# Kernel tuning notes

Measured on AMD Instinct MI355X. Metric: run time of the kernel, lower is better.

Reference implementation:

```python
import jax, jax.numpy as jnp
import numpy as np

T, A, F, E_FEAT = 64, 16, 4, 64
E = F * E_FEAT          # 256 lattice embed dim
H_ENC = 256             # encoder LSTM hidden (per direction)
D_IN = 256              # input token embed dim
DEC_HID = 2 * H_ENC     # decoder hidden = concat(fwd,bwd) encoder hidden
D_ATTN = 256
V_LAT, V_IN = 20000, 100000
NEG = jnp.float32(-1e10)
DEC_LAYERS = 2


def setup_inputs() -> dict:
    key = jax.random.key(0)
    ks = jax.random.split(key, 20)
    def gn(k, shape, scale=0.05):
        return jax.random.normal(k, shape, dtype=jnp.float32) * scale
    inp = {}
    inp['lattice'] = jax.random.randint(ks[0], (1, T, A, F), 0, V_LAT, dtype=jnp.int32)
    inp['analysis_lengths'] = jnp.full((1, T), A, dtype=jnp.int32)
    inp['inputs'] = jax.random.randint(ks[1], (1, T), 0, V_IN, dtype=jnp.int32)
    inp['input_lengths'] = jnp.full((1, 1, 1), T, dtype=jnp.int32)
    inp['gold_indices'] = jax.random.randint(ks[2], (1, T), 0, A, dtype=jnp.int32)
    inp['sos_ids'] = jax.random.randint(ks[3], (F,), 0, V_LAT, dtype=jnp.int32)
    inp['lat_emb_table'] = gn(ks[4], (V_LAT, E_FEAT))
    inp['in_emb_table'] = gn(ks[5], (V_IN, D_IN))
    # encoder biLSTM: 2 layers x 2 directions (PyTorch gate order i,f,g,o)
    inp['enc_Wih0'] = gn(ks[6], (2, 4 * H_ENC, E))
    inp['enc_Whh0'] = gn(ks[7], (2, 4 * H_ENC, H_ENC))
    inp['enc_b0'] = gn(ks[8], (2, 4 * H_ENC))
    inp['enc_Wih1'] = gn(ks[9], (2, 4 * H_ENC, 2 * H_ENC))
    inp['enc_Whh1'] = gn(ks[10], (2, 4 * H_ENC, H_ENC))
    inp['enc_b1'] = gn(ks[11], (2, 4 * H_ENC))
    # decoder LSTM: 2 layers, input = E + D_IN == DEC_HID
    inp['dec_Wih'] = gn(ks[12], (DEC_LAYERS, 4 * DEC_HID, E + D_IN))
    inp['dec_Whh'] = gn(ks[13], (DEC_LAYERS, 4 * DEC_HID, DEC_HID))
    inp['dec_b'] = gn(ks[14], (DEC_LAYERS, 4 * DEC_HID))
    # additive pointer attention
    inp['attn_Wq'] = gn(ks[15], (DEC_HID, D_ATTN))
    inp['attn_Wk'] = gn(ks[16], (DEC_HID, D_ATTN))
    inp['attn_v'] = gn(ks[17], (D_ATTN,))
    return inp


def _lstm_cell(x, h, c, Wih, Whh, b):
    g = x @ Wih.T + h @ Whh.T + b
    i, f, gg, o = jnp.split(g, 4, axis=-1)
    c = jax.nn.sigmoid(f) * c + jax.nn.sigmoid(i) * jnp.tanh(gg)
    h = jax.nn.sigmoid(o) * jnp.tanh(c)
    return h, c


def _lstm_layer(xs, Wih, Whh, b, reverse):
    h0 = jnp.zeros((Whh.shape[-1],), xs.dtype)
    def step(carry, x):
        h, c = _lstm_cell(x, carry[0], carry[1], Wih, Whh, b)
        return (h, c), h
    (hT, cT), ys = jax.lax.scan(step, (h0, h0), xs, reverse=reverse)
    return ys, hT, cT


def reference(lattice, analysis_lengths, inputs, input_lengths, gold_indices, sos_ids,
              lat_emb_table, in_emb_table,
              enc_Wih0, enc_Whh0, enc_b0, enc_Wih1, enc_Whh1, enc_b1,
              dec_Wih, dec_Whh, dec_b, attn_Wq, attn_Wk, attn_v):
    # embed lattice: per-feature lookup, flatten feature embeds -> [1,T,A,E]
    emb_lat = lat_emb_table[lattice].reshape(1, T, A, E)
    # pack full lattice (analysis_lengths == A) into one sequence [T*A, E]
    x = emb_lat[0].reshape(T * A, E)
    # encoder biLSTM layer 0
    yf, hf0, cf0 = _lstm_layer(x, enc_Wih0[0], enc_Whh0[0], enc_b0[0], False)
    yb, hb0, cb0 = _lstm_layer(x, enc_Wih0[1], enc_Whh0[1], enc_b0[1], True)
    y = jnp.concatenate([yf, yb], axis=-1)
    # encoder biLSTM layer 1
    yf, hf1, cf1 = _lstm_layer(y, enc_Wih1[0], enc_Whh1[0], enc_b1[0], False)
    yb, hb1, cb1 = _lstm_layer(y, enc_Wih1[1], enc_Whh1[1], enc_b1[1], True)
    enc = jnp.concatenate([yf, yb], axis=-1).reshape(T, A, DEC_HID)
    # decoder init hidden: concat fwd/bwd final states per layer (matches the
    # view/transpose/reshape in forward_lattice_encode)
    h_dec = jnp.stack([jnp.concatenate([hf0, hb0]), jnp.concatenate([hf1, hb1])])
    c_dec = jnp.stack([jnp.concatenate([cf0, cb0]), jnp.concatenate([cf1, cb1])])
    sos_emb = lat_emb_table[sos_ids].reshape(E)
    tok_emb = in_emb_table[inputs[0]]      # [T, D_IN]
    lat_seq = emb_lat[0]                   # [T, A, E]
    gold = gold_indices[0]                 # [T] teacher forcing
    alens = analysis_lengths[0]            # [T]
    col = jnp.arange(A)

    def step(carry, xs):
        h, c, prev = carry
        enc_t, tok_t, lat_t, g_t, len_t = xs
        inp_t = jnp.concatenate([prev, tok_t])   # [E + D_IN]
        hs, cs = [], []
        for l in range(DEC_LAYERS):
            hl, cl = _lstm_cell(inp_t, h[l], c[l], dec_Wih[l], dec_Whh[l], dec_b[l])
            hs.append(hl); cs.append(cl)
            inp_t = hl
        att = jnp.tanh(enc_t @ attn_Wk + inp_t @ attn_Wq) @ attn_v   # [A]
        scores = jnp.where(col < len_t, att, NEG)
        return (jnp.stack(hs), jnp.stack(cs), lat_t[g_t]), scores

    _, scores = jax.lax.scan(step, (h_dec, c_dec, sos_emb), (enc, tok_emb, lat_seq, gold, alens))
    return scores[None]  # [1, T, A]
```

## Files before the change

### kernel.cpp

```cpp
#include <hip/hip_runtime.h>
#include <math.h>

#define T_STEPS 64
#define A_DIM   16
#define SEQ     1024
#define HE      256
#define DH      512
#define GE      1024
#define GD      2048

typedef _Float16 h2_t __attribute__((ext_vector_type(2)));

__device__ __forceinline__ float sigf(float x) { return 1.f / (1.f + __expf(-x)); }
__device__ __forceinline__ float tanh_fast(float x) {
    float e = __expf(-2.f * x);
    return (1.f - e) / (1.f + e);
}

__device__ __forceinline__ float fdot2f(h2_t a, h2_t b, float c) {
#if defined(__has_builtin) && __has_builtin(__builtin_amdgcn_fdot2)
    return __builtin_amdgcn_fdot2(a, b, c, false);
#else
    return c + (float)a.x * (float)b.x + (float)a.y * (float)b.y;
#endif
}

__device__ __forceinline__ float poll_comm(const float* p) {
    float v;
    do {
        v = __hip_atomic_load(p, __ATOMIC_RELAXED, __HIP_MEMORY_SCOPE_AGENT);
    } while (v == 0.f);
    return v - 4.0f;
}

__device__ __forceinline__ void post_comm(float* p, float h) {
    __hip_atomic_store(p, h + 4.0f, __ATOMIC_RELAXED, __HIP_MEMORY_SCOPE_AGENT);
}

__global__ void k_embed(const int* __restrict__ lattice, const int* __restrict__ inputs,
                        const int* __restrict__ gold, const int* __restrict__ sos,
                        const float* __restrict__ lat_emb, const float* __restrict__ in_emb,
                        float* __restrict__ x, float* __restrict__ decin)
{
    int idx = blockIdx.x * 256 + threadIdx.x;
    if (idx < SEQ * 256) {
        int row = idx >> 8, e = idx & 255;
        int f = e >> 6, eo = e & 63;
        int id = lattice[row * 4 + f];
        x[idx] = lat_emb[id * 64 + eo];
    } else {
        int k = idx - SEQ * 256;
        if (k < T_STEPS * 512) {
            int t = k >> 9, d = k & 511;
            float val;
            if (d < 256) {
                int f = d >> 6, eo = d & 63;
                int id = (t == 0) ? sos[f]
                                  : lattice[(((t - 1) * A_DIM) + gold[t - 1]) * 4 + f];
                val = lat_emb[id * 64 + eo];
            } else {
                val = in_emb[inputs[t] * 256 + (d - 256)];
            }
            decin[k] = val;
        }
    }
}

__global__ __launch_bounds__(256) void k_gemm(
    const float* __restrict__ A, int lda, long sA,
    const float* __restrict__ B, int ldbn, int ldbk, long sB,
    const float* __restrict__ bias, int sBias,
    float* __restrict__ C, int ldc, long sC,
    int M, int N, int K)
{
    int b = blockIdx.z;
    A += b * sA; B += b * sB; C += b * sC;
    if (bias) bias += (long)b * sBias;
    int n0 = blockIdx.x * 64, m0 = blockIdx.y * 64;
    __shared__ float As[64][17];
    __shared__ float Bs[64][17];
    int tid = threadIdx.x;
    int tn = tid & 15, tm = tid >> 4;
    float acc[4][4] = {};
    int lk = tid & 15, lr = tid >> 4;
    for (int k0 = 0; k0 < K; k0 += 16) {
#pragma unroll
        for (int i = 0; i < 4; i++) {
            int row = lr + i * 16;
            int am = m0 + row;
            As[row][lk] = (am < M) ? A[(long)am * lda + k0 + lk] : 0.f;
            int bn = n0 + row;
            Bs[row][lk] = (bn < N) ? B[(long)bn * ldbn + (long)(k0 + lk) * ldbk] : 0.f;
        }
        __syncthreads();
#pragma unroll
        for (int k = 0; k < 16; k++) {
            float av[4], bv[4];
#pragma unroll
            for (int i = 0; i < 4; i++) av[i] = As[tm * 4 + i][k];
#pragma unroll
            for (int j = 0; j < 4; j++) bv[j] = Bs[tn * 4 + j][k];
#pragma unroll
            for (int i = 0; i < 4; i++)
#pragma unroll
                for (int j = 0; j < 4; j++) acc[i][j] += av[i] * bv[j];
        }
        __syncthreads();
    }
#pragma unroll
    for (int i = 0; i < 4; i++) {
        int m = m0 + tm * 4 + i;
        if (m >= M) continue;
#pragma unroll
        for (int j = 0; j < 4; j++) {
            int n = n0 + tn * 4 + j;
            if (n < N) C[(long)m * ldc + n] = acc[i][j] + (bias ? bias[n] : 0.f);
        }
    }
}

__global__ __launch_bounds__(256, 1) void k_rec_enc(
    const float* __restrict__ pre,
    const float* __restrict__ Whh,
    float* __restrict__ y,
    float* __restrict__ hfin,
    float* __restrict__ cfin,
    float* __restrict__ comm)
{
    const int tid = threadIdx.x, bid = blockIdx.x;
    const int r = bid & 3, dir = bid >> 2;
    const bool fwd = (dir == 0);
    const int jj = tid & 63, j = r * 64 + jj;
    const int row = (tid >> 6) * HE + j;
    const float* pre_d = pre + (long)dir * SEQ * GE;
    float* comm_d = comm + (long)dir * SEQ * HE;

    h2_t w2[128];
    {
        const float4* wr = (const float4*)(Whh + (long)dir * GE * HE + (long)row * HE);
#pragma unroll
        for (int i = 0; i < 64; i++) {
            float4 v = wr[i];
            w2[2 * i]     = h2_t{(_Float16)v.x, (_Float16)v.y};
            w2[2 * i + 1] = h2_t{(_Float16)v.z, (_Float16)v.w};
        }
    }

    __shared__ __align__(16) _Float16 hsArr[HE];
    __shared__ float gl[256];
    hsArr[tid] = (_Float16)0.f;
    __syncthreads();

    float c = 0.f, h_cur = 0.f;
    float pre_cur = pre_d[(long)(fwd ? 0 : SEQ - 1) * GE + row];

    for (int s = 0; s < SEQ; s++) {
        const int t = fwd ? s : SEQ - 1 - s;
        float acc = 0.f;
        const float4* hv = (const float4*)hsArr;
#pragma unroll
        for (int kk = 0; kk < 32; kk++) {
            float4 blk = hv[kk];
            const h2_t* hp = (const h2_t*)&blk;
            acc = fdot2f(w2[4 * kk + 0], hp[0], acc);
            acc = fdot2f(w2[4 * kk + 1], hp[1], acc);
            acc = fdot2f(w2[4 * kk + 2], hp[2], acc);
            acc = fdot2f(w2[4 * kk + 3], hp[3], acc);
        }
        gl[tid] = pre_cur + acc;
        if (s + 1 < SEQ) pre_cur = pre_d[(long)(fwd ? t + 1 : t - 1) * GE + row];
        __syncthreads();
        if (tid < 64) {
            float gi = gl[jj], gf = gl[64 + jj], gg = gl[128 + jj], go = gl[192 + jj];
            c = sigf(gf) * c + sigf(gi) * tanh_fast(gg);
            h_cur = sigf(go) * tanh_fast(c);
            post_comm(&comm_d[(long)t * HE + j], h_cur);
            y[(long)t * 512 + dir * HE + j] = h_cur;
            hsArr[j] = (_Float16)h_cur;
        }
        if (s + 1 < SEQ && tid < 192) {
            int idx = (r * 64 + 64 + tid) & 255;
            hsArr[idx] = (_Float16)poll_comm(&comm_d[(long)t * HE + idx]);
        }
        __syncthreads();
    }
    if (tid < 64) {
        hfin[dir * HE + j] = h_cur;
        cfin[dir * HE + j] = c;
    }
}

__global__ __launch_bounds__(256, 1) void k_rec_dec(
    const float* __restrict__ pre,
    const float* __restrict__ Whh,
    const float* __restrict__ hinit,
    const float* __restrict__ cinit,
    float* __restrict__ hseq,
    float* __restrict__ comm)
{
    const int tid = threadIdx.x, r = blockIdx.x;
    const int kh = tid >> 7, rem = tid & 127;
    const int q = rem >> 5, jj = rem & 31;
    const int row = q * DH + r * 32 + jj;
    const int k0 = kh * 256;

    h2_t w2[128];
    {
        const float4* wr = (const float4*)(Whh + (long)row * DH + k0);
#pragma unroll
        for (int i = 0; i < 64; i++) {
            float4 v = wr[i];
            w2[2 * i]     = h2_t{(_Float16)v.x, (_Float16)v.y};
            w2[2 * i + 1] = h2_t{(_Float16)v.z, (_Float16)v.w};
        }
    }

    __shared__ __align__(16) _Float16 hsArr[DH];
    __shared__ float part[256];
    __shared__ float gate[128];
    hsArr[tid] = (_Float16)hinit[tid];
    hsArr[tid + 256] = (_Float16)hinit[tid + 256];
    float c = (tid < 32) ? cinit[r * 32 + tid] : 0.f;
    float pre_cur = (tid < 128) ? pre[row] : 0.f;
    float h_cur = 0.f;
    __syncthreads();

    for (int s = 0; s < T_STEPS; s++) {
        float acc = 0.f;
        const float4* hv = (const float4*)(hsArr + k0);
#pragma unroll
        for (int kk = 0; kk < 32; kk++) {
            float4 blk = hv[kk];
            const h2_t* hp = (const h2_t*)&blk;
            acc = fdot2f(w2[4 * kk + 0], hp[0], acc);
            acc = fdot2f(w2[4 * kk + 1], hp[1], acc);
            acc = fdot2f(w2[4 * kk + 2], hp[2], acc);
            acc = fdot2f(w2[4 * kk + 3], hp[3], acc);
        }
        part[tid] = acc;
        __syncthreads();
        if (tid < 128) {
            float g = part[tid] + part[tid + 128] + pre_cur;
            if (s + 1 < T_STEPS) pre_cur = pre[(long)(s + 1) * GD + row];
            gate[tid] = g;
        }
        __syncthreads();
        if (tid < 32) {
            int jg = r * 32 + tid;
            float gi = gate[tid], gf = gate[32 + tid], gg = gate[64 + tid], go = gate[96 + tid];
            c = sigf(gf) * c + sigf(gi) * tanh_fast(gg);
            h_cur = sigf(go) * tanh_fast(c);
            post_comm(&comm[(long)s * DH + jg], h_cur);
            hseq[(long)s * DH + jg] = h_cur;
            hsArr[jg] = (_Float16)h_cur;
        }
        if (s + 1 < T_STEPS) {
            if (tid < 224) {
                int idx = (r * 32 + 32 + tid) & 511;
                hsArr[idx] = (_Float16)poll_comm(&comm[(long)s * DH + idx]);
            }
            {
                int idx = (r * 32 + 256 + tid) & 511;
                hsArr[idx] = (_Float16)poll_comm(&comm[(long)s * DH + idx]);
            }
        }
        __syncthreads();
    }
}

__global__ void k_attn(const float* __restrict__ encK, const float* __restrict__ qs,
                       const float* __restrict__ v, const int* __restrict__ alens,
                       float* __restrict__ out)
{
    int t = blockIdx.x;
    int tid = threadIdx.x;
    int wave = tid >> 6, lane = tid & 63;
    int len = alens[t];
    const float* qt = qs + t * 256;
    for (int a = wave; a < A_DIM; a += 4) {
        const float* ek = encK + (long)(t * A_DIM + a) * 256;
        float sum = 0.f;
#pragma unroll
        for (int e = 0; e < 4; e++) {
            int d = lane * 4 + e;
            sum += v[d] * tanhf(ek[d] + qt[d]);
        }
        for (int off = 32; off; off >>= 1) sum += __shfl_down(sum, off, 64);
        if (lane == 0) out[t * A_DIM + a] = (a < len) ? sum : -1e10f;
    }
}

extern "C" void kernel_launch(void* const* d_in, const int* in_sizes, int n_in,
                              void* d_out, int out_size, void* d_ws, size_t ws_size,
                              hipStream_t stream)
{
    (void)in_sizes; (void)n_in; (void)out_size; (void)ws_size;
    const int*   lattice = (const int*)d_in[0];
    const int*   alens   = (const int*)d_in[1];
    const int*   inputs  = (const int*)d_in[2];
    const int*   gold    = (const int*)d_in[4];
    const int*   sos     = (const int*)d_in[5];
    const float* lat_emb = (const float*)d_in[6];
    const float* in_emb  = (const float*)d_in[7];
    const float* Wih0    = (const float*)d_in[8];
    const float* Whh0    = (const float*)d_in[9];
    const float* b0      = (const float*)d_in[10];
    const float* Wih1    = (const float*)d_in[11];
    const float* Whh1    = (const float*)d_in[12];
    const float* b1      = (const float*)d_in[13];
    const float* dWih    = (const float*)d_in[14];
    const float* dWhh    = (const float*)d_in[15];
    const float* db      = (const float*)d_in[16];
    const float* Wq      = (const float*)d_in[17];
    const float* Wk      = (const float*)d_in[18];
    const float* av      = (const float*)d_in[19];
    float* out = (float*)d_out;
    float* ws  = (float*)d_ws;

    float* comm  = ws;
    float* commD = ws + 524288;
    float* xbuf  = ws + 589824;
    float* dpre  = xbuf;
    float* h0seq = xbuf + 131072;
    float* h1seq = xbuf + 163840;
    float* qseq  = xbuf + 196608;
    float* pre   = ws + 851968;
    float* y0    = ws + 2949120;
    float* hdec  = ws + 3473408;
    float* cdec  = ws + 3474432;
    float* decin = ws + 3475456;
    float* encK  = ws + 3508224;

    hipMemsetAsync(ws, 0, (524288 + 65536) * sizeof(float), stream);

    k_embed<<<1152, 256, 0, stream>>>(lattice, inputs, gold, sos, lat_emb, in_emb, xbuf, decin);

    k_gemm<<<dim3(16, 16, 2), 256, 0, stream>>>(
        xbuf, 256, 0L, Wih0, 256, 1, (long)GE * 256, b0, GE,
        pre, GE, (long)SEQ * GE, SEQ, GE, 256);
    k_rec_enc<<<8, 256, 0, stream>>>(pre, Whh0, y0, hdec, cdec, comm);

    hipMemsetAsync(comm, 0, 524288 * sizeof(float), stream);

    k_gemm<<<dim3(16, 16, 2), 256, 0, stream>>>(
        y0, 512, 0L, Wih1, 512, 1, (long)GE * 512, b1, GE,
        pre, GE, (long)SEQ * GE, SEQ, GE, 512);
    k_rec_enc<<<8, 256, 0, stream>>>(pre, Whh1, y0, hdec + 512, cdec + 512, comm);

    k_gemm<<<dim3(4, 16, 1), 256, 0, stream>>>(
        y0, 512, 0L, Wk, 1, 256, 0L, nullptr, 0,
        encK, 256, 0L, SEQ, 256, 512);

    k_gemm<<<dim3(32, 1, 1), 256, 0, stream>>>(
        decin, 512, 0L, dWih, 512, 1, 0L, db, 0,
        dpre, GD, 0L, T_STEPS, GD, 512);
    k_rec_dec<<<16, 256, 0, stream>>>(dpre, dWhh, hdec, cdec, h0seq, commD);

    k_gemm<<<dim3(32, 1, 1), 256, 0, stream>>>(
        h0seq, 512, 0L, dWih + (long)GD * 512, 512, 1, 0L, db + GD, 0,
        dpre, GD, 0L, T_STEPS, GD, 512);
    k_rec_dec<<<16, 256, 0, stream>>>(dpre, dWhh + (long)GD * 512, hdec + 512, cdec + 512,
                                      h1seq, commD + 32768);

    k_gemm<<<dim3(4, 1, 1), 256, 0, stream>>>(
        h1seq, 512, 0L, Wq, 1, 256, 0L, nullptr, 0,
        qseq, 256, 0L, T_STEPS, 256, 512);

    k_attn<<<64, 256, 0, stream>>>(encK, qseq, av, alens, out);
}
```

Before: 3.964 ms.

## Run each encoder LSTM direction in one 1024-thread block, dropping cross-block polling

Measured after the change: 6.673 ms. 1.68x slower.

```diff
diff --git a/kernel.cpp b/kernel.cpp
--- a/kernel.cpp
+++ b/kernel.cpp
@@ -1,5 +1,6 @@
 #include <hip/hip_runtime.h>
 #include <math.h>
+#include <stdint.h>
 
 #define T_STEPS 64
 #define A_DIM   16
@@ -119,47 +120,54 @@
     }
 }
 
-__global__ __launch_bounds__(256, 1) void k_rec_enc(
+__global__ __launch_bounds__(1024) void k_rec_enc(
     const float* __restrict__ pre,
     const float* __restrict__ Whh,
     float* __restrict__ y,
     float* __restrict__ hfin,
-    float* __restrict__ cfin,
-    float* __restrict__ comm)
-{
-    const int tid = threadIdx.x, bid = blockIdx.x;
-    const int r = bid & 3, dir = bid >> 2;
+    float* __restrict__ cfin)
+{
+    const int tid = threadIdx.x;
+    const int dir = blockIdx.x;
     const bool fwd = (dir == 0);
-    const int jj = tid & 63, j = r * 64 + jj;
-    const int row = (tid >> 6) * HE + j;
-    const float* pre_d = pre + (long)dir * SEQ * GE;
-    float* comm_d = comm + (long)dir * SEQ * HE;
-
-    h2_t w2[128];
+    const int g = tid & 3, j = tid >> 2;
+    const int row = g * HE + j;
+    const float* pre_d = pre + (size_t)dir * SEQ * GE;
+
+    __shared__ h2_t LDSW[36 * 1024];
+    __shared__ __align__(16) _Float16 hbuf[2][HE];
+
+    h2_t w2[92];
     {
-        const float4* wr = (const float4*)(Whh + (long)dir * GE * HE + (long)row * HE);
-#pragma unroll
-        for (int i = 0; i < 64; i++) {
+        const float4* wr = (const float4*)(Whh + (size_t)dir * GE * HE + (size_t)row * HE);
+#pragma unroll
+        for (int i = 0; i < 46; i++) {
             float4 v = wr[i];
             w2[2 * i]     = h2_t{(_Float16)v.x, (_Float16)v.y};
             w2[2 * i + 1] = h2_t{(_Float16)v.z, (_Float16)v.w};
         }
-    }
-
-    __shared__ __align__(16) _Float16 hsArr[HE];
-    __shared__ float gl[256];
-    hsArr[tid] = (_Float16)0.f;
+        for (int i = 46; i < 64; i++) {
+            float4 v = wr[i];
+            LDSW[(2 * i - 92) * 1024 + tid] = h2_t{(_Float16)v.x, (_Float16)v.y};
+            LDSW[(2 * i - 91) * 1024 + tid] = h2_t{(_Float16)v.z, (_Float16)v.w};
+        }
+    }
+    if (tid < HE) { hbuf[0][tid] = (_Float16)0.f; hbuf[1][tid] = (_Float16)0.f; }
     __syncthreads();
 
     float c = 0.f, h_cur = 0.f;
-    float pre_cur = pre_d[(long)(fwd ? 0 : SEQ - 1) * GE + row];
+    float pre_cur = pre_d[(size_t)(fwd ? 0 : SEQ - 1) * GE + row];
+    const int qbase = (tid & 63) & ~3;
 
     for (int s = 0; s < SEQ; s++) {
         const int t = fwd ? s : SEQ - 1 - s;
+        float pre_nxt = 0.f;
+        if (s + 1 < SEQ) pre_nxt = pre_d[(size_t)(fwd ? t + 1 : t - 1) * GE + row];
+
         float acc = 0.f;
-        const float4* hv = (const float4*)hsArr;
-#pragma unroll
-        for (int kk = 0; kk < 32; kk++) {
+        const float4* hv = (const float4*)hbuf[s & 1];
+#pragma unroll
+        for (int kk = 0; kk < 23; kk++) {
             float4 blk = hv[kk];
             const h2_t* hp = (const h2_t*)&blk;
             acc = fdot2f(w2[4 * kk + 0], hp[0], acc);
@@ -167,24 +175,30 @@
             acc = fdot2f(w2[4 * kk + 2], hp[2], acc);
             acc = fdot2f(w2[4 * kk + 3], hp[3], acc);
         }
-        gl[tid] = pre_cur + acc;
-        if (s + 1 < SEQ) pre_cur = pre_d[(long)(fwd ? t + 1 : t - 1) * GE + row];
-        __syncthreads();
-        if (tid < 64) {
-            float gi = gl[jj], gf = gl[64 + jj], gg = gl[128 + jj], go = gl[192 + jj];
-            c = sigf(gf) * c + sigf(gi) * tanh_fast(gg);
-            h_cur = sigf(go) * tanh_fast(c);
-            post_comm(&comm_d[(long)t * HE + j], h_cur);
-            y[(long)t * 512 + dir * HE + j] = h_cur;
-            hsArr[j] = (_Float16)h_cur;
-        }
-        if (s + 1 < SEQ && tid < 192) {
-            int idx = (r * 64 + 64 + tid) & 255;
-            hsArr[idx] = (_Float16)poll_comm(&comm_d[(long)t * HE + idx]);
-        }
-        __syncthreads();
-    }
-    if (tid < 64) {
+#pragma unroll
+        for (int cc = 0; cc < 9; cc++) {
+            float4 blk = hv[23 + cc];
+            const h2_t* hp = (const h2_t*)&blk;
+#pragma unroll
+            for (int e = 0; e < 4; e++)
+                acc = fdot2f(LDSW[(4 * cc + e) * 1024 + tid], hp[e], acc);
+        }
+
+        float gval = pre_cur + acc;
+        pre_cur = pre_nxt;
+        float gi = __shfl(gval, qbase + 0, 64);
+        float gf = __shfl(gval, qbase + 1, 64);
+        float gg = __shfl(gval, qbase + 2, 64);
+        float go = __shfl(gval, qbase + 3, 64);
+        c = sigf(gf) * c + sigf(gi) * tanh_fast(gg);
+        h_cur = sigf(go) * tanh_fast(c);
+        if (g == 0) {
+            y[(size_t)t * 512 + dir * HE + j] = h_cur;
+            hbuf[(s + 1) & 1][j] = (_Float16)h_cur;
+        }
+        __syncthreads();
+    }
+    if (g == 0) {
         hfin[dir * HE + j] = h_cur;
         cfin[dir * HE + j] = c;
     }
@@ -330,22 +344,21 @@
     float* cdec  = ws + 3474432;
     float* decin = ws + 3475456;
     float* encK  = ws + 3508224;
-
-    hipMemsetAsync(ws, 0, (524288 + 65536) * sizeof(float), stream);
+    (void)comm;
+
+    hipMemsetAsync(commD, 0, 65536 * sizeof(float), stream);
 
     k_embed<<<1152, 256, 0, stream>>>(lattice, inputs, gold, sos, lat_emb, in_emb, xbuf, decin);
 
     k_gemm<<<dim3(16, 16, 2), 256, 0, stream>>>(
         xbuf, 256, 0L, Wih0, 256, 1, (long)GE * 256, b0, GE,
         pre, GE, (long)SEQ * GE, SEQ, GE, 256);
-    k_rec_enc<<<8, 256, 0, stream>>>(pre, Whh0, y0, hdec, cdec, comm);
-
-    hipMemsetAsync(comm, 0, 524288 * sizeof(float), stream);
+    k_rec_enc<<<2, 1024, 0, stream>>>(pre, Whh0, y0, hdec, cdec);
 
     k_gemm<<<dim3(16, 16, 2), 256, 0, stream>>>(
         y0, 512, 0L, Wih1, 512, 1, (long)GE * 512, b1, GE,
         pre, GE, (long)SEQ * GE, SEQ, GE, 512);
-    k_rec_enc<<<8, 256, 0, stream>>>(pre, Whh1, y0, hdec + 512, cdec + 512, comm);
+    k_rec_enc<<<2, 1024, 0, stream>>>(pre, Whh1, y0, hdec + 512, cdec + 512);
 
     k_gemm<<<dim3(4, 16, 1), 256, 0, stream>>>(
         y0, 512, 0L, Wk, 1, 256, 0L, nullptr, 0,
```
